# Kernel optimization log

Measured on AMD Instinct MI355X. Metric: run time of the kernel, lower is better.

## Reference

```python
import jax, jax.numpy as jnp
import numpy as np

# dims: NL layers, D=d_model, DI=expand*D, F=d_ff, V=vocab, L=S*C seq, R=dt_rank, N=d_state, K=d_conv
NL, D, DI, F, V, L, R, N, K = 2, 256, 512, 1024, 1024, 1024, 16, 16, 4
B, S, C = 2, 128, 8
EPS = 1e-5


def silu(x):
    return x * jax.nn.sigmoid(x)


def batchnorm(x, g, b):  # x: [B,L,D], normalize over (B,L) per channel (training-mode BatchNorm1d)
    m = x.mean((0, 1))
    v = x.var((0, 1))
    return (x - m) * jax.lax.rsqrt(v + EPS) * g + b


def layernorm(x, g, b):
    m = x.mean(-1, keepdims=True)
    v = x.var(-1, keepdims=True)
    return (x - m) * jax.lax.rsqrt(v + EPS) * g + b


def mamba(x, Win, cw, cb, Wx, Wdt, bdt, A_log, Dsk, Wout, bout):
    # x: [B,L,D] -> [B,L,D]; standard Mamba block with selective scan
    Bsz, Lseq, _ = x.shape
    xz = x @ Win                      # [B,L,2*DI]
    xi, z = jnp.split(xz, 2, axis=-1)
    # depthwise causal conv1d, width K
    xp = jnp.pad(xi, ((0, 0), (K - 1, 0), (0, 0)))
    xc = cb + sum(xp[:, k:k + Lseq, :] * cw[:, k] for k in range(K))
    xc = silu(xc)                     # [B,L,DI]
    xdb = xc @ Wx                     # [B,L,R+2N]
    delta = jax.nn.softplus(xdb[..., :R] @ Wdt + bdt)   # [B,L,DI]
    Bm = xdb[..., R:R + N]            # [B,L,N]
    Cm = xdb[..., R + N:]             # [B,L,N]
    A = -jnp.exp(A_log)               # [DI,N]
    dA = jnp.exp(delta[..., None] * A)                       # [B,L,DI,N]
    dBx = delta[..., None] * Bm[:, :, None, :] * xc[..., None]  # [B,L,DI,N]

    def step(h, inp):
        dA_t, dBx_t, C_t = inp
        h = h * dA_t + dBx_t          # [B,DI,N]
        y = jnp.einsum('bdn,bn->bd', h, C_t)
        return h, y

    h0 = jnp.zeros((Bsz, DI, N), x.dtype)
    _, ys = jax.lax.scan(step, h0, (dA.transpose(1, 0, 2, 3), dBx.transpose(1, 0, 2, 3), Cm.transpose(1, 0, 2)))
    y = ys.transpose(1, 0, 2) + Dsk * xc
    y = y * silu(z)
    return y @ Wout + bout


def _forward(input_ids, emb, pos, Win, conv_w, conv_b, Wx, Wdt, bdt, A_log, Dskip, Wout, bout,
             bn_g, bn_b, ln_g, ln_b, ff_w1, ff_b1, ff_w2, ff_b2, final_w, final_b):
    Bsz, Ssz, Csz = input_ids.shape
    Lseq = Ssz * Csz
    # Encoder: token embedding (scaled) + learned positions, flattened to [B, S*C, D]
    x = emb[input_ids].reshape(Bsz, Lseq, D) * jnp.sqrt(jnp.float32(D)) + pos[:Lseq]
    for i in range(NL):
        f = mamba(x, Win[i, 0], conv_w[i, 0], conv_b[i, 0], Wx[i, 0], Wdt[i, 0], bdt[i, 0],
                  A_log[i, 0], Dskip[i, 0], Wout[i, 0], bout[i, 0])
        f = batchnorm(f, bn_g[i, 0], bn_b[i, 0])
        bk = mamba(x[:, ::-1], Win[i, 1], conv_w[i, 1], conv_b[i, 1], Wx[i, 1], Wdt[i, 1], bdt[i, 1],
                   A_log[i, 1], Dskip[i, 1], Wout[i, 1], bout[i, 1])
        bk = batchnorm(bk, bn_g[i, 1], bn_b[i, 1])[:, ::-1]
        f = layernorm(x + f, ln_g[i, 0], ln_b[i, 0])
        bk = layernorm(x + bk, ln_g[i, 1], ln_b[i, 1])
        out = f + bk
        out = jax.nn.relu(out @ ff_w1[i] + ff_b1[i]) @ ff_w2[i] + ff_b2[i]
        out = batchnorm(out, bn_g[i, 2], bn_b[i, 2])
        x = out + x
    return x.reshape(Bsz, Ssz, Csz, D) @ final_w + final_b   # [B,S,C,V]


def setup_inputs() -> dict:
    key = jax.random.key(0)
    ks = list(jax.random.split(key, 16))
    kit = iter(ks)
    rn = lambda shape, s=0.02: jax.random.normal(next(kit), shape, jnp.float32) * s
    inp = {
        'input_ids': jax.random.randint(next(kit), (B, S, C), 0, V),
        'emb': rn((V, D)), 'pos': rn((L, D)),
        'Win': rn((NL, 2, D, 2 * DI)),
        'conv_w': rn((NL, 2, DI, K), 0.1), 'conv_b': jnp.zeros((NL, 2, DI)),
        'Wx': rn((NL, 2, DI, R + 2 * N)),
        'Wdt': rn((NL, 2, R, DI)), 'bdt': jnp.full((NL, 2, DI), -4.0),
        'A_log': jnp.broadcast_to(jnp.log(jnp.arange(1, N + 1, dtype=jnp.float32)), (NL, 2, DI, N)) + 0.0,
        'Dskip': jnp.ones((NL, 2, DI)),
        'Wout': rn((NL, 2, DI, D)), 'bout': jnp.zeros((NL, 2, D)),
        'bn_g': jnp.ones((NL, 3, D)), 'bn_b': jnp.zeros((NL, 3, D)),
        'ln_g': jnp.ones((NL, 2, D)), 'ln_b': jnp.zeros((NL, 2, D)),
        'ff_w1': rn((NL, D, F)), 'ff_b1': jnp.zeros((NL, F)),
        'ff_w2': rn((NL, F, D)), 'ff_b2': jnp.zeros((NL, D)),
        'final_w': rn((D, V)), 'final_b': jnp.zeros((V,)),
    }
    return inp


def reference(input_ids, emb, pos, Win, conv_w, conv_b, Wx, Wdt, bdt, A_log, Dskip, Wout, bout,
              bn_g, bn_b, ln_g, ln_b, ff_w1, ff_b1, ff_w2, ff_b2, final_w, final_b):
    return _forward(input_ids, emb, pos, Win, conv_w, conv_b, Wx, Wdt, bdt, A_log, Dskip, Wout, bout,
                    bn_g, bn_b, ln_g, ln_b, ff_w1, ff_b1, ff_w2, ff_b2, final_w, final_b)
```

## Files before the change

### kernel.cpp

```cpp
#include <hip/hip_runtime.h>

#define NL 2
#define DMODEL 256
#define DI 512
#define FF 1024
#define VV 1024
#define LSEQ 1024
#define RR 16
#define NN 16
#define KCONV 4
#define BTOK 2048
#define EPS 1e-5f

using short8 = __attribute__((ext_vector_type(8))) short;
using float4v = __attribute__((ext_vector_type(4))) float;
typedef unsigned short u16;

__device__ inline float bf2f(u16 u) {
    union { unsigned u; float f; } x; x.u = (unsigned)u << 16; return x.f;
}
__device__ inline u16 f2bf(float f) {
    union { float f; unsigned u; } x; x.f = f;
    unsigned r = x.u + 0x7fffu + ((x.u >> 16) & 1u);
    return (u16)(r >> 16);
}

#if __has_builtin(__builtin_amdgcn_exp2f)
#define EXP2(x) __builtin_amdgcn_exp2f(x)
#else
#define EXP2(x) exp2f(x)
#endif

struct TMat { const float* src; u16* dst; int rows, cols, tile0, tilecols; };
struct TTable { TMat m[24]; int nmat; };

__global__ __launch_bounds__(256) void transpose_kernel(TTable tt) {
    __shared__ u16 tile[32][33];
    int bx = blockIdx.x;
    int j = 0;
    for (int k = 1; k < tt.nmat; ++k) if (bx >= tt.m[k].tile0) j = k;
    TMat mm = tt.m[j];
    int lt = bx - mm.tile0;
    int r0 = (lt / mm.tilecols) * 32, c0 = (lt % mm.tilecols) * 32;
    int tx = threadIdx.x & 31, ty = threadIdx.x >> 5;
    #pragma unroll
    for (int k = 0; k < 4; ++k) {
        int r = r0 + ty + k * 8, c = c0 + tx;
        tile[ty + k * 8][tx] = (r < mm.rows && c < mm.cols) ? f2bf(mm.src[(size_t)r * mm.cols + c]) : (u16)0;
    }
    __syncthreads();
    #pragma unroll
    for (int k = 0; k < 4; ++k) {
        int c = c0 + ty + k * 8, r = r0 + tx;
        if (c < mm.cols && r < mm.rows) mm.dst[(size_t)c * mm.rows + r] = tile[tx][ty + k * 8];
    }
}

template<int BM, int BN, int WR, int WC, int RT, int CT>
__global__ __launch_bounds__(256) void sgemm_kernel(
    const u16* __restrict__ A0, int lda, unsigned long long sA,
    const u16* __restrict__ B0, int ldb, unsigned long long sB,
    const float* __restrict__ bias0, unsigned long long sBias,
    void* __restrict__ C0, int ldc, unsigned long long sC,
    int K, int act, int outfp, float* __restrict__ stats, int statsStride)
{
    constexpr int BK = 32;
    __shared__ u16 As[BM * BK];
    __shared__ u16 Bs[BN * BK];
    const u16* A = A0 + (size_t)blockIdx.z * sA;
    const u16* Bt = B0 + (size_t)blockIdx.z * sB;
    const float* bias = bias0 ? (bias0 + (size_t)blockIdx.z * sBias) : nullptr;

    const int tid = threadIdx.x, w = tid >> 6, lane = tid & 63;
    const int row0 = blockIdx.y * BM, col0 = blockIdx.x * BN;
    const int wr = w / WC, wc = w % WC;
    const int mi = lane & 15, kq = lane >> 4;
    const int lr = lane >> 2, lc = (lane & 3) * 8;

    float4v acc[RT][CT];
    #pragma unroll
    for (int i = 0; i < RT; ++i)
        #pragma unroll
        for (int j = 0; j < CT; ++j) acc[i][j] = (float4v){0.f, 0.f, 0.f, 0.f};

    for (int kk = 0; kk < K; kk += BK) {
        __syncthreads();
        for (int i = w; i < BM / 16; i += 4) {
            const u16* g = A + (size_t)(row0 + i * 16 + lr) * lda + kk + lc;
            __builtin_amdgcn_global_load_lds(
                (const __attribute__((address_space(1))) void*)g,
                (__attribute__((address_space(3))) void*)(As + i * 16 * BK), 16, 0, 0);
        }
        for (int i = w; i < BN / 16; i += 4) {
            const u16* g = Bt + (size_t)(col0 + i * 16 + lr) * ldb + kk + lc;
            __builtin_amdgcn_global_load_lds(
                (const __attribute__((address_space(1))) void*)g,
                (__attribute__((address_space(3))) void*)(Bs + i * 16 * BK), 16, 0, 0);
        }
        __syncthreads();
        short8 af[RT], bf[CT];
        #pragma unroll
        for (int i = 0; i < RT; ++i)
            af[i] = *(const short8*)(As + (wr * RT * 16 + i * 16 + mi) * BK + kq * 8);
        #pragma unroll
        for (int j = 0; j < CT; ++j)
            bf[j] = *(const short8*)(Bs + (wc * CT * 16 + j * 16 + mi) * BK + kq * 8);
        #pragma unroll
        for (int i = 0; i < RT; ++i)
            #pragma unroll
            for (int j = 0; j < CT; ++j)
                acc[i][j] = __builtin_amdgcn_mfma_f32_16x16x32_bf16(af[i], bf[j], acc[i][j], 0, 0, 0);
    }

    #pragma unroll
    for (int j = 0; j < CT; ++j) {
        const int n = col0 + wc * CT * 16 + j * 16 + mi;
        const float bv = bias ? bias[n] : 0.f;
        float s = 0.f, q = 0.f;
        #pragma unroll
        for (int i = 0; i < RT; ++i) {
            #pragma unroll
            for (int r = 0; r < 4; ++r) {
                int m = row0 + wr * RT * 16 + i * 16 + kq * 4 + r;
                float v = acc[i][j][r] + bv;
                if (act == 1) v = fmaxf(v, 0.f);
                if (outfp)
                    ((float*)C0)[(size_t)blockIdx.z * sC + (size_t)m * ldc + n] = v;
                else
                    ((u16*)C0)[(size_t)blockIdx.z * sC + (size_t)m * ldc + n] = f2bf(v);
                s += v; q += v * v;
            }
        }
        if (stats) {
            s += __shfl_xor(s, 16); s += __shfl_xor(s, 32);
            q += __shfl_xor(q, 16); q += __shfl_xor(q, 32);
            if (lane < 16) {
                atomicAdd(&stats[(size_t)(blockIdx.z * statsStride + n) * 2], s);
                atomicAdd(&stats[(size_t)(blockIdx.z * statsStride + n) * 2 + 1], q);
            }
        }
    }
}

__global__ __launch_bounds__(256) void gemm_kernel(
    const u16* __restrict__ A0, int lda, unsigned long long sA,
    const u16* __restrict__ B0, int ldb, unsigned long long sB,
    const float* __restrict__ bias0, unsigned long long sBias,
    void* __restrict__ C0, int ldc, unsigned long long sC,
    int M, int N, int K, int act, int outfp, u16* __restrict__ bcT0)
{
    const u16* A = A0 + (size_t)blockIdx.z * sA;
    const u16* Bt = B0 + (size_t)blockIdx.z * sB;
    const float* bias = bias0 ? (bias0 + (size_t)blockIdx.z * sBias) : nullptr;

    int tid = threadIdx.x;
    int wv = tid >> 6, lane = tid & 63;
    int row0 = blockIdx.y * 64 + (wv >> 1) * 32;
    int col0 = blockIdx.x * 64 + (wv & 1) * 32;
    int mi = lane & 15, kq = lane >> 4;

    float4v acc[2][2];
    #pragma unroll
    for (int a = 0; a < 2; ++a)
        #pragma unroll
        for (int b = 0; b < 2; ++b) acc[a][b] = (float4v){0.f, 0.f, 0.f, 0.f};
    const short8 zer = {0, 0, 0, 0, 0, 0, 0, 0};

    for (int kk = 0; kk < K; kk += 32) {
        int k = kk + kq * 8;
        bool kv = (k < K);
        short8 af[2], bf[2];
        #pragma unroll
        for (int rt = 0; rt < 2; ++rt) {
            int r = row0 + rt * 16 + mi;
            af[rt] = kv ? *(const short8*)(A + (size_t)r * lda + k) : zer;
        }
        #pragma unroll
        for (int ct = 0; ct < 2; ++ct) {
            int n = col0 + ct * 16 + mi;
            bf[ct] = (kv && n < N) ? *(const short8*)(Bt + (size_t)n * ldb + k) : zer;
        }
        #pragma unroll
        for (int rt = 0; rt < 2; ++rt)
            #pragma unroll
            for (int ct = 0; ct < 2; ++ct)
                acc[rt][ct] = __builtin_amdgcn_mfma_f32_16x16x32_bf16(af[rt], bf[ct], acc[rt][ct], 0, 0, 0);
    }

    #pragma unroll
    for (int rt = 0; rt < 2; ++rt)
        #pragma unroll
        for (int ct = 0; ct < 2; ++ct) {
            int n = col0 + ct * 16 + mi;
            if (n >= N) continue;
            float bv = bias ? bias[n] : 0.f;
            #pragma unroll
            for (int r = 0; r < 4; ++r) {
                int m = row0 + rt * 16 + kq * 4 + r;
                float v = acc[rt][ct][r] + bv;
                if (act == 1) v = fmaxf(v, 0.f);
                u16 hv = f2bf(v);
                if (outfp)
                    ((float*)C0)[(size_t)blockIdx.z * sC + (size_t)m * ldc + n] = v;
                else
                    ((u16*)C0)[(size_t)blockIdx.z * sC + (size_t)m * ldc + n] = hv;
                if (bcT0 && n >= 16) {
                    int bb = m >> 10, t = m & 1023;
                    bcT0[((size_t)((blockIdx.z * 2 + bb) * 32 + (n - 16))) * LSEQ + t] = hv;
                }
            }
        }
}

__global__ __launch_bounds__(256) void delta_fused_kernel(
    const u16* __restrict__ xdb, const u16* __restrict__ wdtT,
    const float* __restrict__ bdt, const u16* __restrict__ xc,
    u16* __restrict__ deltaT, u16* __restrict__ uT, int layer)
{
    int z = blockIdx.z;
    const u16* A = xdb + (size_t)z * BTOK * 48;
    const u16* Bt = wdtT + (size_t)z * 512 * 16;
    const float* bias = bdt + (size_t)z * 512;

    int tid = threadIdx.x;
    int wv = tid >> 6, lane = tid & 63;
    int row0 = blockIdx.y * 64 + (wv >> 1) * 32;
    int col0 = blockIdx.x * 64 + (wv & 1) * 32;
    int mi = lane & 15, kq = lane >> 4;

    float4v acc[2][2];
    #pragma unroll
    for (int a = 0; a < 2; ++a)
        #pragma unroll
        for (int b = 0; b < 2; ++b) acc[a][b] = (float4v){0.f, 0.f, 0.f, 0.f};
    const short8 zer = {0, 0, 0, 0, 0, 0, 0, 0};

    int k = kq * 8;
    bool kv = (k < 16);
    short8 af[2], bf[2];
    #pragma unroll
    for (int rt = 0; rt < 2; ++rt) {
        int r = row0 + rt * 16 + mi;
        af[rt] = kv ? *(const short8*)(A + (size_t)r * 48 + k) : zer;
    }
    #pragma unroll
    for (int ct = 0; ct < 2; ++ct) {
        int n = col0 + ct * 16 + mi;
        bf[ct] = kv ? *(const short8*)(Bt + (size_t)n * 16 + k) : zer;
    }
    #pragma unroll
    for (int rt = 0; rt < 2; ++rt)
        #pragma unroll
        for (int ct = 0; ct < 2; ++ct)
            acc[rt][ct] = __builtin_amdgcn_mfma_f32_16x16x32_bf16(af[rt], bf[ct], acc[rt][ct], 0, 0, 0);

    #pragma unroll
    for (int rt = 0; rt < 2; ++rt)
        #pragma unroll
        for (int ct = 0; ct < 2; ++ct) {
            int n = col0 + ct * 16 + mi;
            float bv = bias[n];
            #pragma unroll
            for (int r = 0; r < 4; ++r) {
                int m = row0 + rt * 16 + kq * 4 + r;
                float v = acc[rt][ct][r] + bv;
                v = (v > 20.f) ? v : logf(1.f + __expf(v));
                float xcv = bf2f(xc[((size_t)z * BTOK + m) * DI + n]);
                int b = m >> 10, t = m & 1023;
                size_t off = ((size_t)((z * 2 + b) * DI + n)) * LSEQ + t;
                deltaT[off] = f2bf(v);
                uT[off] = f2bf(v * xcv);
            }
        }
}

__global__ __launch_bounds__(256) void embed_kernel(
    const int* __restrict__ ids, const float* __restrict__ emb,
    const float* __restrict__ pos, u16* __restrict__ x)
{
    int tok = blockIdx.x, d = threadIdx.x;
    int id = ids[tok];
    float v = emb[(size_t)id * DMODEL + d] * 16.0f + pos[(size_t)(tok & (LSEQ - 1)) * DMODEL + d];
    x[(size_t)tok * DMODEL + d] = f2bf(v);
}

__global__ __launch_bounds__(256) void conv_kernel(
    const u16* __restrict__ xz, const float* __restrict__ conv_w,
    const float* __restrict__ conv_b, u16* __restrict__ xc, int layer)
{
    unsigned g = blockIdx.x * 256u + threadIdx.x;
    int d = g & 511;
    int t = (g >> 9) & 1023;
    int b = (g >> 19) & 1;
    int dir = g >> 20;
    int wbase = ((layer * 2 + dir) * DI + d);
    float acc = conv_b[wbase];
    int colbase = dir * 1024 + d;
    #pragma unroll
    for (int k = 0; k < KCONV; ++k) {
        int ts = dir ? (t + 3 - k) : (t - 3 + k);
        if (ts >= 0 && ts < LSEQ)
            acc += conv_w[wbase * KCONV + k] * bf2f(xz[(size_t)((b << 10) + ts) * 2048 + colbase]);
    }
    float v = acc / (1.f + __expf(-acc));
    xc[(size_t)(((dir * 2 + b) << 10) + t) * DI + d] = f2bf(v);
}

template<int DIR>
__device__ __forceinline__ void scan_body(
    const u16* __restrict__ deltaT, const u16* __restrict__ uT,
    const u16* __restrict__ bcT, const float* __restrict__ A_log,
    u16* __restrict__ pT, int layer, int slab,
    float* Ps, float* Qs)
{
    const int c = threadIdx.x;
    const int d = blockIdx.x;

    float a2[16];
    const float* al = A_log + (size_t)(((layer * 2 + DIR) * DI + d) * NN);
    #pragma unroll
    for (int n = 0; n < 16; ++n) a2[n] = -__expf(al[n]) * 1.44269504f;

    const size_t tb = ((size_t)(slab * DI + d)) * LSEQ;
    const size_t bcb = (size_t)slab * 32 * LSEQ;
    const int T0 = DIR ? (1016 - 8 * c) : (8 * c);

    short8 dlv = *(const short8*)(deltaT + tb + T0);
    short8 uvv = *(const short8*)(uT + tb + T0);
    float dls[8], uvs[8];
    #pragma unroll
    for (int s = 0; s < 8; ++s) {
        const int idx = DIR ? 7 - s : s;
        dls[s] = bf2f((u16)dlv[idx]);
        uvs[s] = bf2f((u16)uvv[idx]);
    }

    const int base = c * 17;
    #pragma unroll
    for (int n = 0; n < 16; ++n) {
        short8 B8 = *(const short8*)(bcT + bcb + (size_t)n * LSEQ + T0);
        float P = 1.f, Q = 0.f;
        #pragma unroll
        for (int s = 0; s < 8; ++s) {
            const int idx = DIR ? 7 - s : s;
            float dA = EXP2(dls[s] * a2[n]);
            Q = Q * dA + uvs[s] * bf2f((u16)B8[idx]);
            P *= dA;
        }
        Ps[base + n] = P;
        Qs[base + n] = Q;
    }
    __syncthreads();

    for (int off = 1; off < 128; off <<= 1) {
        float np[16], nq[16];
        const bool act = (c >= off);
        if (act) {
            const int nb = (c - off) * 17;
            #pragma unroll
            for (int n = 0; n < 16; ++n) { np[n] = Ps[nb + n]; nq[n] = Qs[nb + n]; }
        }
        __syncthreads();
        if (act) {
            #pragma unroll
            for (int n = 0; n < 16; ++n) {
                float p = Ps[base + n], q = Qs[base + n];
                Qs[base + n] = fmaf(p, nq[n], q);
                Ps[base + n] = p * np[n];
            }
        }
        __syncthreads();
    }

    float pacc[8];
    #pragma unroll
    for (int s = 0; s < 8; ++s) pacc[s] = 0.f;
    const int hb = (c - 1) * 17;
    #pragma unroll
    for (int n = 0; n < 16; ++n) {
        short8 B8 = *(const short8*)(bcT + bcb + (size_t)n * LSEQ + T0);
        short8 C8 = *(const short8*)(bcT + bcb + (size_t)(16 + n) * LSEQ + T0);
        float h = (c == 0) ? 0.f : Qs[hb + n];
        #pragma unroll
        for (int s = 0; s < 8; ++s) {
            const int idx = DIR ? 7 - s : s;
            float dA = EXP2(dls[s] * a2[n]);
            h = h * dA + uvs[s] * bf2f((u16)B8[idx]);
            pacc[s] = fmaf(h, bf2f((u16)C8[idx]), pacc[s]);
        }
    }
    short8 pk;
    #pragma unroll
    for (int s = 0; s < 8; ++s) {
        const int idx = DIR ? 7 - s : s;
        pk[idx] = (short)f2bf(pacc[s]);
    }
    *(short8*)(pT + tb + T0) = pk;
}

__global__ __launch_bounds__(128) void scan_kernel(
    const u16* __restrict__ deltaT, const u16* __restrict__ uT,
    const u16* __restrict__ bcT, const float* __restrict__ A_log,
    u16* __restrict__ pT, int layer)
{
    __shared__ float Ps[128 * 17], Qs[128 * 17];
    int slab = blockIdx.y;
    if (slab >> 1)
        scan_body<1>(deltaT, uT, bcT, A_log, pT, layer, slab, Ps, Qs);
    else
        scan_body<0>(deltaT, uT, bcT, A_log, pT, layer, slab, Ps, Qs);
}

__global__ __launch_bounds__(256) void gate_kernel(
    const u16* __restrict__ pT, const u16* __restrict__ xc,
    const u16* __restrict__ xz, const float* __restrict__ Dskip,
    u16* __restrict__ y, float* __restrict__ statsM, int layer)
{
    if (blockIdx.x == 0 && blockIdx.y == 0 && blockIdx.z == 0) {
        for (int k = threadIdx.x; k < 2048; k += 256) statsM[k] = 0.f;
    }
    __shared__ float tile[32][33];
    int z = blockIdx.z, dir = z >> 1, b = z & 1;
    int d0 = blockIdx.x * 32, t0 = blockIdx.y * 32;
    int tx = threadIdx.x & 31, ty = threadIdx.x >> 5;
    #pragma unroll
    for (int k = 0; k < 4; ++k) {
        int d = d0 + ty + k * 8;
        tile[ty + k * 8][tx] = bf2f(pT[((size_t)(z * DI + d)) * LSEQ + t0 + tx]);
    }
    __syncthreads();
    #pragma unroll
    for (int k = 0; k < 4; ++k) {
        int t = t0 + ty + k * 8, d = d0 + tx;
        float p = tile[tx][ty + k * 8];
        float xcv = bf2f(xc[(size_t)((z << 10) + t) * DI + d]);
        float zv = bf2f(xz[(size_t)((b << 10) + t) * 2048 + dir * 1024 + 512 + d]);
        float dsk = Dskip[(layer * 2 + dir) * DI + d];
        float yv = (p + dsk * xcv) * (zv / (1.f + __expf(-zv)));
        y[(size_t)((z << 10) + t) * DI + d] = f2bf(yv);
    }
}

__global__ __launch_bounds__(256) void fuseln_kernel(
    const u16* __restrict__ x, const u16* __restrict__ outm, const float* __restrict__ stats,
    const float* __restrict__ bng, const float* __restrict__ bnb,
    const float* __restrict__ lng, const float* __restrict__ lnb,
    u16* __restrict__ ffin, float* __restrict__ statsF)
{
    int tok = blockIdx.x, d = threadIdx.x;
    if (tok == 0) { for (int k = d; k < 512; k += 256) statsF[k] = 0.f; }
    float xv = bf2f(x[(size_t)tok * DMODEL + d]);
    float of = bf2f(outm[(size_t)tok * DMODEL + d]);
    float ob = bf2f(outm[(size_t)BTOK * DMODEL + (size_t)tok * DMODEL + d]);
    float mf0 = stats[d * 2] * (1.f / 2048.f);
    float rf0 = rsqrtf(stats[d * 2 + 1] * (1.f / 2048.f) - mf0 * mf0 + EPS);
    float mb0 = stats[(DMODEL + d) * 2] * (1.f / 2048.f);
    float rb0 = rsqrtf(stats[(DMODEL + d) * 2 + 1] * (1.f / 2048.f) - mb0 * mb0 + EPS);
    float vf = xv + (of - mf0) * rf0 * bng[d] + bnb[d];
    float vb = xv + (ob - mb0) * rb0 * bng[DMODEL + d] + bnb[DMODEL + d];
    float s0 = vf, s1 = vf * vf, s2 = vb, s3 = vb * vb;
    #pragma unroll
    for (int off = 1; off < 64; off <<= 1) {
        s0 += __shfl_xor(s0, off); s1 += __shfl_xor(s1, off);
        s2 += __shfl_xor(s2, off); s3 += __shfl_xor(s3, off);
    }
    __shared__ float sm[4][4];
    if ((d & 63) == 0) { sm[d >> 6][0] = s0; sm[d >> 6][1] = s1; sm[d >> 6][2] = s2; sm[d >> 6][3] = s3; }
    __syncthreads();
    s0 = sm[0][0] + sm[1][0] + sm[2][0] + sm[3][0];
    s1 = sm[0][1] + sm[1][1] + sm[2][1] + sm[3][1];
    s2 = sm[0][2] + sm[1][2] + sm[2][2] + sm[3][2];
    s3 = sm[0][3] + sm[1][3] + sm[2][3] + sm[3][3];
    float mf = s0 * (1.f / 256.f), vvf = s1 * (1.f / 256.f) - mf * mf;
    float mb = s2 * (1.f / 256.f), vvb = s3 * (1.f / 256.f) - mb * mb;
    float fl = (vf - mf) * rsqrtf(vvf + EPS) * lng[d] + lnb[d];
    float bl = (vb - mb) * rsqrtf(vvb + EPS) * lng[DMODEL + d] + lnb[DMODEL + d];
    ffin[(size_t)tok * DMODEL + d] = f2bf(fl + bl);
}

__global__ __launch_bounds__(256) void bnadd_kernel(
    u16* __restrict__ x, const u16* __restrict__ ffo, const float* __restrict__ stats,
    const float* __restrict__ g, const float* __restrict__ b)
{
    int tok = blockIdx.x, d = threadIdx.x;
    size_t idx = (size_t)tok * DMODEL + d;
    float mean = stats[d * 2] * (1.f / 2048.f);
    float rs = rsqrtf(stats[d * 2 + 1] * (1.f / 2048.f) - mean * mean + EPS);
    float v = bf2f(x[idx]) + (bf2f(ffo[idx]) - mean) * rs * g[d] + b[d];
    x[idx] = f2bf(v);
}

extern "C" void kernel_launch(void* const* d_in, const int* in_sizes, int n_in,
                              void* d_out, int out_size, void* d_ws, size_t ws_size,
                              hipStream_t stream)
{
    const int*   ids     = (const int*)d_in[0];
    const float* emb     = (const float*)d_in[1];
    const float* pos     = (const float*)d_in[2];
    const float* Win     = (const float*)d_in[3];
    const float* conv_w  = (const float*)d_in[4];
    const float* conv_b  = (const float*)d_in[5];
    const float* Wx      = (const float*)d_in[6];
    const float* Wdt     = (const float*)d_in[7];
    const float* bdt     = (const float*)d_in[8];
    const float* A_log   = (const float*)d_in[9];
    const float* Dskip   = (const float*)d_in[10];
    const float* Wout    = (const float*)d_in[11];
    const float* bout    = (const float*)d_in[12];
    const float* bn_g    = (const float*)d_in[13];
    const float* bn_b    = (const float*)d_in[14];
    const float* ln_g    = (const float*)d_in[15];
    const float* ln_b    = (const float*)d_in[16];
    const float* ff_w1   = (const float*)d_in[17];
    const float* ff_b1   = (const float*)d_in[18];
    const float* ff_w2   = (const float*)d_in[19];
    const float* ff_b2   = (const float*)d_in[20];
    const float* final_w = (const float*)d_in[21];
    const float* final_b = (const float*)d_in[22];

    char* cur = (char*)d_ws;
    auto alloc = [&](size_t elems) {
        u16* p = (u16*)cur;
        cur += ((elems * 2 + 511) / 512) * 512;
        return p;
    };
    u16* winT  = alloc((size_t)NL * 2048 * 256);
    u16* wxT   = alloc((size_t)NL * 2 * 48 * 512);
    u16* wdtT  = alloc((size_t)NL * 2 * 512 * 16);
    u16* woutT = alloc((size_t)NL * 2 * 256 * 512);
    u16* fw1T  = alloc((size_t)NL * 1024 * 256);
    u16* fw2T  = alloc((size_t)NL * 256 * 1024);
    u16* finT  = alloc((size_t)1024 * 256);
    u16* xbuf   = alloc((size_t)BTOK * DMODEL);
    u16* xz     = alloc((size_t)BTOK * 2048);
    u16* xc     = alloc((size_t)2 * BTOK * DI);
    u16* xdb    = alloc((size_t)2 * BTOK * 48);
    u16* bcT    = alloc((size_t)4 * 32 * LSEQ);
    u16* deltaT = alloc((size_t)2 * BTOK * DI);
    u16* uT     = alloc((size_t)2 * BTOK * DI);
    u16* pT     = alloc((size_t)2 * BTOK * DI);
    u16* ybuf   = alloc((size_t)2 * BTOK * DI);
    u16* outm   = alloc((size_t)2 * BTOK * DMODEL);
    u16* ffin   = alloc((size_t)BTOK * DMODEL);
    u16* ffh    = alloc((size_t)BTOK * FF);
    u16* ffo    = alloc((size_t)BTOK * DMODEL);
    float* statsM = (float*)alloc(4096);
    float* statsF = statsM + 2048;

    TTable tt; int nm = 0, tiles = 0;
    auto addT = [&](const float* src, u16* dst, int rows, int cols) {
        int tc = (cols + 31) / 32, tr = (rows + 31) / 32;
        tt.m[nm] = {src, dst, rows, cols, tiles, tc};
        tiles += tc * tr; nm++;
    };
    for (int i = 0; i < NL; ++i) {
        for (int dir = 0; dir < 2; ++dir) {
            addT(Win  + (size_t)(i * 2 + dir) * 256 * 1024, winT  + (size_t)i * 2048 * 256 + (size_t)dir * 1024 * 256, 256, 1024);
            addT(Wx   + (size_t)(i * 2 + dir) * 512 * 48,   wxT   + (size_t)(i * 2 + dir) * 48 * 512,   512, 48);
            addT(Wdt  + (size_t)(i * 2 + dir) * 16 * 512,   wdtT  + (size_t)(i * 2 + dir) * 512 * 16,   16, 512);
            addT(Wout + (size_t)(i * 2 + dir) * 512 * 256,  woutT + (size_t)(i * 2 + dir) * 256 * 512,  512, 256);
        }
        addT(ff_w1 + (size_t)i * 256 * 1024, fw1T + (size_t)i * 1024 * 256, 256, 1024);
        addT(ff_w2 + (size_t)i * 1024 * 256, fw2T + (size_t)i * 256 * 1024, 1024, 256);
    }
    addT(final_w, finT, 256, 1024);
    tt.nmat = nm;
    transpose_kernel<<<tiles, 256, 0, stream>>>(tt);

    embed_kernel<<<BTOK, 256, 0, stream>>>(ids, emb, pos, xbuf);

    for (int i = 0; i < NL; ++i) {
        sgemm_kernel<128, 128, 2, 2, 4, 4><<<dim3(16, 16), 256, 0, stream>>>(
            xbuf, 256, 0ULL, winT + (size_t)i * 2048 * 256, 256, 0ULL, nullptr, 0ULL,
            xz, 2048, 0ULL, 256, 0, 0, nullptr, 0);
        conv_kernel<<<(2 * BTOK * DI) / 256, 256, 0, stream>>>(xz, conv_w, conv_b, xc, i);
        gemm_kernel<<<dim3(1, 32, 2), 256, 0, stream>>>(
            xc, 512, (unsigned long long)((size_t)BTOK * 512),
            wxT + (size_t)i * 2 * 48 * 512, 512, 48ULL * 512, nullptr, 0ULL,
            xdb, 48, (unsigned long long)((size_t)BTOK * 48), BTOK, 48, 512, 0, 0, bcT);
        delta_fused_kernel<<<dim3(8, 32, 2), 256, 0, stream>>>(
            xdb, wdtT + (size_t)i * 2 * 512 * 16, bdt + (size_t)i * 2 * 512, xc, deltaT, uT, i);
        scan_kernel<<<dim3(512, 4), 128, 0, stream>>>(deltaT, uT, bcT, A_log, pT, i);
        gate_kernel<<<dim3(DI / 32, LSEQ / 32, 4), 256, 0, stream>>>(pT, xc, xz, Dskip, ybuf, statsM, i);
        sgemm_kernel<64, 64, 2, 2, 2, 2><<<dim3(4, 32, 2), 256, 0, stream>>>(
            ybuf, 512, (unsigned long long)((size_t)BTOK * 512),
            woutT + (size_t)i * 2 * 256 * 512, 512, 256ULL * 512,
            bout + (size_t)i * 2 * 256, 256ULL,
            outm, 256, (unsigned long long)((size_t)BTOK * 256), 512, 0, 0, statsM, 256);
        fuseln_kernel<<<BTOK, 256, 0, stream>>>(xbuf, outm, statsM,
            bn_g + (size_t)i * 3 * 256, bn_b + (size_t)i * 3 * 256,
            ln_g + (size_t)i * 2 * 256, ln_b + (size_t)i * 2 * 256, ffin, statsF);
        sgemm_kernel<128, 64, 4, 1, 2, 4><<<dim3(16, 16), 256, 0, stream>>>(
            ffin, 256, 0ULL, fw1T + (size_t)i * 1024 * 256, 256, 0ULL,
            ff_b1 + (size_t)i * 1024, 0ULL, ffh, 1024, 0ULL, 256, 1, 0, nullptr, 0);
        sgemm_kernel<64, 64, 2, 2, 2, 2><<<dim3(4, 32), 256, 0, stream>>>(
            ffh, 1024, 0ULL, fw2T + (size_t)i * 256 * 1024, 1024, 0ULL,
            ff_b2 + (size_t)i * 256, 0ULL, ffo, 256, 0ULL, 1024, 0, 0, statsF, 0);
        bnadd_kernel<<<BTOK, 256, 0, stream>>>(xbuf, ffo, statsF,
            bn_g + (size_t)(i * 3 + 2) * 256, bn_b + (size_t)(i * 3 + 2) * 256);
    }
    sgemm_kernel<128, 64, 4, 1, 2, 4><<<dim3(16, 16), 256, 0, stream>>>(
        xbuf, 256, 0ULL, finT, 256, 0ULL, final_b, 0ULL,
        d_out, 1024, 0ULL, 256, 0, 1, nullptr, 0);
}
```

Measured before the change: 387.8 us.

## Fuse conv, x-projection and delta projection into one per-tile kernel

Replaces the separate conv, xdb GEMM and delta kernels with one kernel per 16-token tile. The tile computes conv+SiLU into shared memory, runs the Wx projection from LDS, keeps the dt part in shared memory, and computes softplus delta and u directly. This removes two launches and the global round trips of xc and xdb. In exchange the grid shrinks to 256 blocks, the conv loop is serial per block, and only 3 of 4 waves do the Wx MFMA; the stats buffer is also enlarged.

```diff
diff --git a/kernel.cpp b/kernel.cpp
--- a/kernel.cpp
+++ b/kernel.cpp
@@ -4,13 +4,12 @@
 #define DMODEL 256
 #define DI 512
 #define FF 1024
-#define VV 1024
 #define LSEQ 1024
-#define RR 16
 #define NN 16
 #define KCONV 4
 #define BTOK 2048
 #define EPS 1e-5f
+#define XCP 520
 
 using short8 = __attribute__((ext_vector_type(8))) short;
 using float4v = __attribute__((ext_vector_type(4))) float;
@@ -142,136 +141,82 @@
     }
 }
 
-__global__ __launch_bounds__(256) void gemm_kernel(
-    const u16* __restrict__ A0, int lda, unsigned long long sA,
-    const u16* __restrict__ B0, int ldb, unsigned long long sB,
-    const float* __restrict__ bias0, unsigned long long sBias,
-    void* __restrict__ C0, int ldc, unsigned long long sC,
-    int M, int N, int K, int act, int outfp, u16* __restrict__ bcT0)
-{
-    const u16* A = A0 + (size_t)blockIdx.z * sA;
-    const u16* Bt = B0 + (size_t)blockIdx.z * sB;
-    const float* bias = bias0 ? (bias0 + (size_t)blockIdx.z * sBias) : nullptr;
-
+__global__ __launch_bounds__(256) void xcdelta_kernel(
+    const u16* __restrict__ xz, const float* __restrict__ conv_w,
+    const float* __restrict__ conv_b, const u16* __restrict__ wxT_l,
+    const u16* __restrict__ wdtT_l, const float* __restrict__ bdt_l,
+    u16* __restrict__ xc, u16* __restrict__ bcT,
+    u16* __restrict__ deltaT, u16* __restrict__ uT, int layer)
+{
+    __shared__ u16 xcs[16 * XCP];
+    __shared__ u16 xdb16[16 * 16];
+    const short8 zer = {0, 0, 0, 0, 0, 0, 0, 0};
+    int vb = blockIdx.x;
+    int dir = vb >> 7, tile = vb & 127;
+    int m0 = tile * 16;
+    int b = m0 >> 10, tbase = m0 & 1023;
     int tid = threadIdx.x;
-    int wv = tid >> 6, lane = tid & 63;
-    int row0 = blockIdx.y * 64 + (wv >> 1) * 32;
-    int col0 = blockIdx.x * 64 + (wv & 1) * 32;
+    int w = tid >> 6, lane = tid & 63;
     int mi = lane & 15, kq = lane >> 4;
 
-    float4v acc[2][2];
-    #pragma unroll
-    for (int a = 0; a < 2; ++a)
-        #pragma unroll
-        for (int b = 0; b < 2; ++b) acc[a][b] = (float4v){0.f, 0.f, 0.f, 0.f};
-    const short8 zer = {0, 0, 0, 0, 0, 0, 0, 0};
-
-    for (int kk = 0; kk < K; kk += 32) {
-        int k = kk + kq * 8;
-        bool kv = (k < K);
-        short8 af[2], bf[2];
-        #pragma unroll
-        for (int rt = 0; rt < 2; ++rt) {
-            int r = row0 + rt * 16 + mi;
-            af[rt] = kv ? *(const short8*)(A + (size_t)r * lda + k) : zer;
-        }
-        #pragma unroll
-        for (int ct = 0; ct < 2; ++ct) {
-            int n = col0 + ct * 16 + mi;
-            bf[ct] = (kv && n < N) ? *(const short8*)(Bt + (size_t)n * ldb + k) : zer;
-        }
-        #pragma unroll
-        for (int rt = 0; rt < 2; ++rt)
-            #pragma unroll
-            for (int ct = 0; ct < 2; ++ct)
-                acc[rt][ct] = __builtin_amdgcn_mfma_f32_16x16x32_bf16(af[rt], bf[ct], acc[rt][ct], 0, 0, 0);
-    }
-
-    #pragma unroll
-    for (int rt = 0; rt < 2; ++rt)
-        #pragma unroll
-        for (int ct = 0; ct < 2; ++ct) {
-            int n = col0 + ct * 16 + mi;
-            if (n >= N) continue;
-            float bv = bias ? bias[n] : 0.f;
-            #pragma unroll
-            for (int r = 0; r < 4; ++r) {
-                int m = row0 + rt * 16 + kq * 4 + r;
-                float v = acc[rt][ct][r] + bv;
-                if (act == 1) v = fmaxf(v, 0.f);
-                u16 hv = f2bf(v);
-                if (outfp)
-                    ((float*)C0)[(size_t)blockIdx.z * sC + (size_t)m * ldc + n] = v;
-                else
-                    ((u16*)C0)[(size_t)blockIdx.z * sC + (size_t)m * ldc + n] = hv;
-                if (bcT0 && n >= 16) {
-                    int bb = m >> 10, t = m & 1023;
-                    bcT0[((size_t)((blockIdx.z * 2 + bb) * 32 + (n - 16))) * LSEQ + t] = hv;
-                }
-            }
-        }
-}
-
-__global__ __launch_bounds__(256) void delta_fused_kernel(
-    const u16* __restrict__ xdb, const u16* __restrict__ wdtT,
-    const float* __restrict__ bdt, const u16* __restrict__ xc,
-    u16* __restrict__ deltaT, u16* __restrict__ uT, int layer)
-{
-    int z = blockIdx.z;
-    const u16* A = xdb + (size_t)z * BTOK * 48;
-    const u16* Bt = wdtT + (size_t)z * 512 * 16;
-    const float* bias = bdt + (size_t)z * 512;
-
-    int tid = threadIdx.x;
-    int wv = tid >> 6, lane = tid & 63;
-    int row0 = blockIdx.y * 64 + (wv >> 1) * 32;
-    int col0 = blockIdx.x * 64 + (wv & 1) * 32;
-    int mi = lane & 15, kq = lane >> 4;
-
-    float4v acc[2][2];
-    #pragma unroll
-    for (int a = 0; a < 2; ++a)
-        #pragma unroll
-        for (int b = 0; b < 2; ++b) acc[a][b] = (float4v){0.f, 0.f, 0.f, 0.f};
-    const short8 zer = {0, 0, 0, 0, 0, 0, 0, 0};
-
-    int k = kq * 8;
-    bool kv = (k < 16);
-    short8 af[2], bf[2];
-    #pragma unroll
-    for (int rt = 0; rt < 2; ++rt) {
-        int r = row0 + rt * 16 + mi;
-        af[rt] = kv ? *(const short8*)(A + (size_t)r * 48 + k) : zer;
-    }
-    #pragma unroll
-    for (int ct = 0; ct < 2; ++ct) {
-        int n = col0 + ct * 16 + mi;
-        bf[ct] = kv ? *(const short8*)(Bt + (size_t)n * 16 + k) : zer;
-    }
-    #pragma unroll
-    for (int rt = 0; rt < 2; ++rt)
-        #pragma unroll
-        for (int ct = 0; ct < 2; ++ct)
-            acc[rt][ct] = __builtin_amdgcn_mfma_f32_16x16x32_bf16(af[rt], bf[ct], acc[rt][ct], 0, 0, 0);
-
-    #pragma unroll
-    for (int rt = 0; rt < 2; ++rt)
-        #pragma unroll
-        for (int ct = 0; ct < 2; ++ct) {
-            int n = col0 + ct * 16 + mi;
-            float bv = bias[n];
-            #pragma unroll
-            for (int r = 0; r < 4; ++r) {
-                int m = row0 + rt * 16 + kq * 4 + r;
-                float v = acc[rt][ct][r] + bv;
-                v = (v > 20.f) ? v : logf(1.f + __expf(v));
-                float xcv = bf2f(xc[((size_t)z * BTOK + m) * DI + n]);
-                int b = m >> 10, t = m & 1023;
-                size_t off = ((size_t)((z * 2 + b) * DI + n)) * LSEQ + t;
-                deltaT[off] = f2bf(v);
-                uT[off] = f2bf(v * xcv);
-            }
-        }
+    for (int e = tid; e < 16 * 512; e += 256) {
+        int row = e >> 9, d = e & 511;
+        int t = tbase + row;
+        int wbase = ((layer * 2 + dir) * DI + d);
+        float acc = conv_b[wbase];
+        int colbase = dir * 1024 + d;
+        #pragma unroll
+        for (int k = 0; k < KCONV; ++k) {
+            int ts = dir ? (t + 3 - k) : (t - 3 + k);
+            if (ts >= 0 && ts < LSEQ)
+                acc += conv_w[wbase * KCONV + k] * bf2f(xz[(size_t)((b << 10) + ts) * 2048 + colbase]);
+        }
+        float v = acc / (1.f + __expf(-acc));
+        u16 hv = f2bf(v);
+        xcs[row * XCP + d] = hv;
+        xc[(size_t)(((dir * 2 + b) << 10) + t) * DI + d] = hv;
+    }
+    __syncthreads();
+
+    if (w < 3) {
+        int n = w * 16 + mi;
+        const u16* Brow = wxT_l + (size_t)dir * 48 * 512 + (size_t)n * 512;
+        float4v acc = (float4v){0.f, 0.f, 0.f, 0.f};
+        for (int kk = 0; kk < 512; kk += 32) {
+            short8 af = *(const short8*)(xcs + mi * XCP + kk + kq * 8);
+            short8 bf = *(const short8*)(Brow + kk + kq * 8);
+            acc = __builtin_amdgcn_mfma_f32_16x16x32_bf16(af, bf, acc, 0, 0, 0);
+        }
+        #pragma unroll
+        for (int rr = 0; rr < 4; ++rr) {
+            int m = kq * 4 + rr;
+            u16 hv = f2bf(acc[rr]);
+            if (w == 0) xdb16[m * 16 + mi] = hv;
+            else bcT[((size_t)((dir * 2 + b) * 32 + (n - 16))) * 1024 + tbase + m] = hv;
+        }
+    }
+    __syncthreads();
+
+    short8 af = (kq < 2) ? *(const short8*)(xdb16 + mi * 16 + kq * 8) : zer;
+    const u16* wdtTd = wdtT_l + (size_t)dir * 512 * 16;
+    const float* biasd = bdt_l + (size_t)dir * 512;
+    #pragma unroll
+    for (int ct = 0; ct < 8; ++ct) {
+        int n = w * 128 + ct * 16 + mi;
+        short8 bf = (kq < 2) ? *(const short8*)(wdtTd + (size_t)n * 16 + kq * 8) : zer;
+        float4v acc = __builtin_amdgcn_mfma_f32_16x16x32_bf16(af, bf,
+                      (float4v){0.f, 0.f, 0.f, 0.f}, 0, 0, 0);
+        #pragma unroll
+        for (int rr = 0; rr < 4; ++rr) {
+            int m = kq * 4 + rr;
+            float v = acc[rr] + biasd[n];
+            v = (v > 20.f) ? v : logf(1.f + __expf(v));
+            float xcv = bf2f(xcs[m * XCP + n]);
+            size_t off = ((size_t)((dir * 2 + b) * 512 + n)) * 1024 + tbase + m;
+            deltaT[off] = f2bf(v);
+            uT[off] = f2bf(v * xcv);
+        }
+    }
 }
 
 __global__ __launch_bounds__(256) void embed_kernel(
@@ -282,28 +227,6 @@
     int id = ids[tok];
     float v = emb[(size_t)id * DMODEL + d] * 16.0f + pos[(size_t)(tok & (LSEQ - 1)) * DMODEL + d];
     x[(size_t)tok * DMODEL + d] = f2bf(v);
-}
-
-__global__ __launch_bounds__(256) void conv_kernel(
-    const u16* __restrict__ xz, const float* __restrict__ conv_w,
-    const float* __restrict__ conv_b, u16* __restrict__ xc, int layer)
-{
-    unsigned g = blockIdx.x * 256u + threadIdx.x;
-    int d = g & 511;
-    int t = (g >> 9) & 1023;
-    int b = (g >> 19) & 1;
-    int dir = g >> 20;
-    int wbase = ((layer * 2 + dir) * DI + d);
-    float acc = conv_b[wbase];
-    int colbase = dir * 1024 + d;
-    #pragma unroll
-    for (int k = 0; k < KCONV; ++k) {
-        int ts = dir ? (t + 3 - k) : (t - 3 + k);
-        if (ts >= 0 && ts < LSEQ)
-            acc += conv_w[wbase * KCONV + k] * bf2f(xz[(size_t)((b << 10) + ts) * 2048 + colbase]);
-    }
-    float v = acc / (1.f + __expf(-acc));
-    xc[(size_t)(((dir * 2 + b) << 10) + t) * DI + d] = f2bf(v);
 }
 
 template<int DIR>
@@ -534,7 +457,6 @@
     u16* xbuf   = alloc((size_t)BTOK * DMODEL);
     u16* xz     = alloc((size_t)BTOK * 2048);
     u16* xc     = alloc((size_t)2 * BTOK * DI);
-    u16* xdb    = alloc((size_t)2 * BTOK * 48);
     u16* bcT    = alloc((size_t)4 * 32 * LSEQ);
     u16* deltaT = alloc((size_t)2 * BTOK * DI);
     u16* uT     = alloc((size_t)2 * BTOK * DI);
@@ -544,7 +466,7 @@
     u16* ffin   = alloc((size_t)BTOK * DMODEL);
     u16* ffh    = alloc((size_t)BTOK * FF);
     u16* ffo    = alloc((size_t)BTOK * DMODEL);
-    float* statsM = (float*)alloc(4096);
+    float* statsM = (float*)alloc(8192);
     float* statsF = statsM + 2048;
 
     TTable tt; int nm = 0, tiles = 0;
@@ -573,13 +495,10 @@
         sgemm_kernel<128, 128, 2, 2, 4, 4><<<dim3(16, 16), 256, 0, stream>>>(
             xbuf, 256, 0ULL, winT + (size_t)i * 2048 * 256, 256, 0ULL, nullptr, 0ULL,
             xz, 2048, 0ULL, 256, 0, 0, nullptr, 0);
-        conv_kernel<<<(2 * BTOK * DI) / 256, 256, 0, stream>>>(xz, conv_w, conv_b, xc, i);
-        gemm_kernel<<<dim3(1, 32, 2), 256, 0, stream>>>(
-            xc, 512, (unsigned long long)((size_t)BTOK * 512),
-            wxT + (size_t)i * 2 * 48 * 512, 512, 48ULL * 512, nullptr, 0ULL,
-            xdb, 48, (unsigned long long)((size_t)BTOK * 48), BTOK, 48, 512, 0, 0, bcT);
-        delta_fused_kernel<<<dim3(8, 32, 2), 256, 0, stream>>>(
-            xdb, wdtT + (size_t)i * 2 * 512 * 16, bdt + (size_t)i * 2 * 512, xc, deltaT, uT, i);
+        xcdelta_kernel<<<256, 256, 0, stream>>>(
+            xz, conv_w, conv_b, wxT + (size_t)i * 2 * 48 * 512,
+            wdtT + (size_t)i * 2 * 512 * 16, bdt + (size_t)i * 2 * 512,
+            xc, bcT, deltaT, uT, i);
         scan_kernel<<<dim3(512, 4), 128, 0, stream>>>(deltaT, uT, bcT, A_log, pT, i);
         gate_kernel<<<dim3(DI / 32, LSEQ / 32, 4), 256, 0, stream>>>(pT, xc, xz, Dskip, ybuf, statsM, i);
         sgemm_kernel<64, 64, 2, 2, 2, 2><<<dim3(4, 32, 2), 256, 0, stream>>>(
```

Result: no change. 393.2 us (+1.4%).
